# Optimization experiments

Measured on AMD Instinct MI355X. Metric: run time of the kernel, lower is better.

Reference implementation:

```python
import jax, jax.numpy as jnp
import numpy as np

K = 16          # neighbors per point
POINTNUM = 2048 # opt.pointnum
B, N = 8, 2048


def _knn_concat(x, k):
    """x: [B,N,C] -> [B,N,k,2C] = concat(center, k-nearest neighbor feats)."""
    sq = jnp.sum(x * x, axis=-1)                                   # [B,N]
    d2 = sq[:, :, None] + sq[:, None, :] - 2.0 * jnp.einsum('bnc,bmc->bnm', x, x)
    _, idx = jax.lax.top_k(-d2, k)                                 # [B,N,k]
    nbr = jax.vmap(lambda xb, ib: xb[ib])(x, idx)                  # [B,N,k,C]
    ctr = jnp.broadcast_to(x[:, :, None, :], nbr.shape)
    return jnp.concatenate([ctr, nbr], axis=-1)


def _lin(x, w, b):
    return x @ w + b


lrelu = jax.nn.leaky_relu  # default negative_slope=0.01 matches nn.LeakyReLU()


def setup_inputs() -> dict:
    key = jax.random.key(0)
    ks = jax.random.split(key, 20)

    def w(k_, fi, fo):
        return jax.random.normal(k_, (fi, fo), jnp.float32) / np.sqrt(fi)

    inp = {
        'x': jax.random.normal(ks[0], (B, N, 3), jnp.float32),
        'h1w1': w(ks[1], 6, 16),   'h1b1': jnp.zeros((16,), jnp.float32),
        'h1w2': w(ks[2], 16, 64),  'h1b2': jnp.zeros((64,), jnp.float32),
        'h1w3': w(ks[3], 64, 32),  'h1b3': jnp.zeros((32,), jnp.float32),
        'h2w1': w(ks[4], 64, 256), 'h2b1': jnp.zeros((256,), jnp.float32),
        'h2w2': w(ks[5], 256, 128),'h2b2': jnp.zeros((128,), jnp.float32),
        'h3w1': w(ks[6], 256, 128),'h3b1': jnp.zeros((128,), jnp.float32),
        'fc1w': w(ks[7], 128, 128),'fc1b': jnp.zeros((128,), jnp.float32),
        'fc2w': w(ks[8], 128, 128),'fc2b': jnp.zeros((128,), jnp.float32),
        'fc3w': w(ks[9], 128, POINTNUM * 3), 'fc3b': jnp.zeros((POINTNUM * 3,), jnp.float32),
    }
    return inp


def reference(x, h1w1, h1b1, h1w2, h1b2, h1w3, h1b3,
              h2w1, h2b1, h2w2, h2b2, h3w1, h3b1,
              fc1w, fc1b, fc2w, fc2b, fc3w, fc3b):
    # block 1: knn-concat [B,N,K,6] -> MLP(6,16,64,32) -> sum over K
    x1 = _knn_concat(x, K)
    h = lrelu(_lin(x1, h1w1, h1b1))
    h = lrelu(_lin(h, h1w2, h1b2))
    h = lrelu(_lin(h, h1w3, h1b3))
    x2 = jnp.sum(h, axis=2)                    # [B,N,32]
    # block 2: [B,N,K,64] -> MLP(64,256,128) -> sum over K
    x2 = _knn_concat(x2, K)
    h = lrelu(_lin(x2, h2w1, h2b1))
    h = lrelu(_lin(h, h2w2, h2b2))
    x3 = jnp.sum(h, axis=2)                    # [B,N,128]
    # block 3: [B,N,K,256] -> MLP(256,128) -> sum over K
    x3 = _knn_concat(x3, K)
    h = lrelu(_lin(x3, h3w1, h3b1))
    x4 = jnp.sum(h, axis=2)                    # [B,N,128]
    # global max pool over points
    x5 = jnp.max(x4, axis=1)                   # [B,128]
    x6 = lrelu(_lin(x5, fc1w, fc1b))
    x7 = lrelu(_lin(x6, fc2w, fc2b))
    x8 = _lin(x7, fc3w, fc3b)                  # [B, POINTNUM*3]
    return x8.reshape(x8.shape[0], POINTNUM, 3)
```

## Files before the change

### kernel.cpp

```cpp
#include <hip/hip_runtime.h>

#define KNB 16
#define BSZ 8
#define NPT 2048

typedef __attribute__((ext_vector_type(8))) short bf16x8;
typedef __attribute__((ext_vector_type(4))) float f32x4;

__device__ __forceinline__ float lrelu(float x) { return x >= 0.f ? x : 0.01f * x; }

__device__ __forceinline__ unsigned short bf16rne(float f) {
    union { float f; unsigned int u; } v; v.f = f;
    return (unsigned short)((v.u + 0x7FFFu + ((v.u >> 16) & 1u)) >> 16);
}

__device__ __forceinline__ float packkey(float d, int idx) {
    union { float f; unsigned int u; } v; v.f = d;
    v.u = (v.u & 0xFFFFF800u) | (unsigned int)idx;
    return v.f;
}

__device__ __forceinline__ void ceA(float& a, float& b) {
    const float lo = fminf(a, b), hi = fmaxf(a, b);
    a = lo; b = hi;
}

__device__ __forceinline__ void bsort16(float* c) {
#pragma unroll
    for (int k = 2; k <= 16; k <<= 1) {
#pragma unroll
        for (int j = k >> 1; j > 0; j >>= 1) {
#pragma unroll
            for (int i = 0; i < 16; ++i) {
                const int l = i ^ j;
                if (l > i) {
                    if ((i & k) == 0) ceA(c[i], c[l]);
                    else              ceA(c[l], c[i]);
                }
            }
        }
    }
}

__device__ __forceinline__ void merge16(float* L, const float* C) {
#pragma unroll
    for (int i = 0; i < 16; ++i) L[i] = fminf(L[i], C[15 - i]);
#pragma unroll
    for (int j = 8; j > 0; j >>= 1) {
#pragma unroll
        for (int i = 0; i < 16; ++i) {
            const int l = i ^ j;
            if (l > i) ceA(L[i], L[l]);
        }
    }
}

__device__ __forceinline__ void st16(float* dst, const float* L) {
#pragma unroll
    for (int c = 0; c < 4; ++c)
        *(f32x4*)(dst + c * 4) = (f32x4){L[c * 4], L[c * 4 + 1], L[c * 4 + 2], L[c * 4 + 3]};
}

__device__ __forceinline__ void ld16(float* L, const float* src) {
#pragma unroll
    for (int c = 0; c < 4; ++c) {
        const f32x4 v = *(const f32x4*)(src + c * 4);
        L[c * 4] = v[0]; L[c * 4 + 1] = v[1]; L[c * 4 + 2] = v[2]; L[c * 4 + 3] = v[3];
    }
}

__device__ __forceinline__ void xwave_merge_out(float (*sS)[20], int w, int lane,
                                                float* L, float* outp) {
    st16(sS[w * 64 + lane], L);
    __syncthreads();
    if ((w & 1) == 0) {
        float C[16];
        ld16(C, sS[(w + 1) * 64 + lane]);
        merge16(L, C);
        if (w == 2) st16(sS[2 * 64 + lane], L);
    }
    __syncthreads();
    if (w == 0) {
        float C[16];
        ld16(C, sS[2 * 64 + lane]);
        merge16(L, C);
        st16(outp, L);
    }
}

__global__ void wprep_kernel(const float* __restrict__ w, unsigned short* __restrict__ wt,
                             int K, int N) {
    int i = blockIdx.x * 256 + threadIdx.x;
    if (i < K * N) { int k = i / N, n = i - k * N; wt[n * K + k] = bf16rne(w[i]); }
}

__global__ void wprep_b1_kernel(const float* __restrict__ w1, const float* __restrict__ w2,
                                const float* __restrict__ w3,
                                unsigned short* __restrict__ w1a, unsigned short* __restrict__ w2a,
                                unsigned short* __restrict__ w3a) {
    int i = blockIdx.x * 256 + threadIdx.x;
    if (i < 512) {
        int n = i >> 5, k = i & 31;
        w1a[i] = (k < 6) ? bf16rne(w1[k * 16 + n]) : (unsigned short)0;
    } else if (i < 2560) {
        int j = i - 512, n = j >> 5, k = j & 31;
        w2a[j] = (k < 16) ? bf16rne(w2[k * 64 + n]) : (unsigned short)0;
    } else if (i < 4608) {
        int j = i - 2560, n = j >> 6, k = j & 63;
        w3a[j] = bf16rne(w3[k * 32 + n]);
    }
}

template<int C>
__global__ void norms16_kernel(const unsigned short* __restrict__ feat, float* __restrict__ out) {
    int gid = blockIdx.x * blockDim.x + threadIdx.x;
    if (gid < BSZ * NPT) {
        const unsigned short* p = feat + (size_t)gid * C;
        float s = 0.f;
#pragma unroll
        for (int c = 0; c < C; ++c) {
            union { unsigned int u; float f; } v; v.u = ((unsigned int)p[c]) << 16;
            s = fmaf(v.f, v.f, s);
        }
        out[gid] = s;
    }
}

template<int C>
__global__ void norms_kernel(const float* __restrict__ feat, float* __restrict__ out) {
    int gid = blockIdx.x * blockDim.x + threadIdx.x;
    if (gid < BSZ * NPT) {
        const float* p = feat + (size_t)gid * C;
        float s = 0.f;
#pragma unroll
        for (int c = 0; c < C; ++c) s = fmaf(p[c], p[c], s);
        out[gid] = s;
    }
}

template<int JS>
__launch_bounds__(256, 3)
__global__ void knn3_kernel(const float* __restrict__ feat,
                            const float* __restrict__ norms,
                            float* __restrict__ cand) {
    constexpr int JL = NPT / JS;
    constexpr int JP = JL / 4;
    const int b = blockIdx.z, js = blockIdx.y, i0 = blockIdx.x * 64;
    const int t = threadIdx.x, w = t >> 6, lane = t & 63;
    const float* fb = feat + (size_t)b * NPT * 3;
    const float* nb = norms + (size_t)b * NPT;

    __shared__ __align__(16) float sS[256][20];

    float q0, q1, q2;
    { const float* qp = fb + (size_t)(i0 + lane) * 3; q0 = qp[0]; q1 = qp[1]; q2 = qp[2]; }

    float L[16];
#pragma unroll
    for (int u = 0; u < 16; ++u) L[u] = 3e38f;

    const int jbeg = js * JL + w * JP;
#pragma unroll 1
    for (int j0 = jbeg; j0 < jbeg + JP; j0 += 16) {
        float C[16];
#pragma unroll
        for (int u = 0; u < 16; ++u) {
            const int j = j0 + u;
            const float* pp = fb + (size_t)j * 3;
            C[u] = packkey(fmaf(-2.f, fmaf(q0, pp[0], fmaf(q1, pp[1], q2 * pp[2])), nb[j]), j);
        }
        bsort16(C);
        merge16(L, C);
    }
    float* o = cand + (((size_t)b * NPT + i0 + lane) * JS + js) * 16;
    xwave_merge_out(sS, w, lane, L, o);
}

template<int C, int JS>
__launch_bounds__(256, 3)
__global__ void knn_mfma_kernel(const unsigned short* __restrict__ fb16,
                                const float* __restrict__ norms,
                                float* __restrict__ cand) {
    constexpr int JL = NPT / JS;
    constexpr int KS = C / 32;
    const int b    = blockIdx.z;
    const int js   = blockIdx.y;
    const int i0   = blockIdx.x * 64;
    const int t    = threadIdx.x;
    const int w    = t >> 6;
    const int lane = t & 63;
    const int l15  = lane & 15;
    const int quad = lane >> 4;
    const unsigned short* fbb = fb16 + (size_t)b * NPT * C;
    const float* nb = norms + (size_t)b * NPT;

    __shared__ __align__(16) float sS[256][20];

    bf16x8 afr[KS * 4];
#pragma unroll
    for (int ks = 0; ks < KS; ++ks)
#pragma unroll
        for (int mi = 0; mi < 4; ++mi)
            afr[ks * 4 + mi] = *(const bf16x8*)(fbb + (size_t)(i0 + mi * 16 + l15) * C + ks * 32 + quad * 8);

    float L[16];
#pragma unroll
    for (int u = 0; u < 16; ++u) L[u] = 3e38f;

    const int jbeg = js * JL;
#pragma unroll 1
    for (int j0 = jbeg; j0 < jbeg + JL; j0 += 64) {
        f32x4 acc[4];
#pragma unroll
        for (int mi = 0; mi < 4; ++mi) acc[mi] = (f32x4){0.f, 0.f, 0.f, 0.f};
        const unsigned short* prow = fbb + (size_t)(j0 + w * 16 + l15) * C + quad * 8;
#pragma unroll
        for (int ks = 0; ks < KS; ++ks) {
            const bf16x8 bfr = *(const bf16x8*)(prow + ks * 32);
#pragma unroll
            for (int mi = 0; mi < 4; ++mi)
                acc[mi] = __builtin_amdgcn_mfma_f32_16x16x32_bf16(afr[ks * 4 + mi], bfr, acc[mi], 0, 0, 0);
        }
        const float nv  = nb[j0 + w * 16 + l15];
        const int  cidx = j0 + w * 16 + l15;
#pragma unroll
        for (int mi = 0; mi < 4; ++mi)
#pragma unroll
            for (int r = 0; r < 4; ++r)
                sS[w * 64 + mi * 16 + quad * 4 + r][l15] = packkey(fmaf(-2.f, acc[mi][r], nv), cidx);
        float Cb[16];
        ld16(Cb, sS[w * 64 + lane]);
        bsort16(Cb);
        merge16(L, Cb);
    }

    float* o = cand + (((size_t)b * NPT + i0 + lane) * JS + js) * 16;
    xwave_merge_out(sS, w, lane, L, o);
}

template<int JS>
__launch_bounds__(256)
__global__ void knn_merge_kernel(const float* __restrict__ cand, int* __restrict__ knn_out) {
    const int q = blockIdx.x * 256 + threadIdx.x;
    const float* pd = cand + (size_t)q * JS * 16;
    float L[16];
    ld16(L, pd);
#pragma unroll
    for (int s = 1; s < JS; ++s) {
        float C[16];
        ld16(C, pd + s * 16);
        merge16(L, C);
    }
    int* o = knn_out + (size_t)q * KNB;
#pragma unroll
    for (int u = 0; u < 16; ++u) {
        union { float f; unsigned int v; } z; z.f = L[u];
        o[u] = (int)(z.v & 2047u);
    }
}

__launch_bounds__(256, 3)
__global__ void block1_mfma_kernel(const float* __restrict__ x, const int* __restrict__ knn,
                                   const unsigned short* __restrict__ w1a, const float* __restrict__ b1,
                                   const unsigned short* __restrict__ w2a, const float* __restrict__ b2,
                                   const unsigned short* __restrict__ w3a, const float* __restrict__ b3,
                                   unsigned short* __restrict__ x2b) {
    const int w = threadIdx.x >> 6, lane = threadIdx.x & 63;
    const int l15 = lane & 15, quad = lane >> 4;

    const bf16x8 W1 = *(const bf16x8*)(w1a + l15 * 32 + quad * 8);
    bf16x8 W2[4];
#pragma unroll
    for (int nt = 0; nt < 4; ++nt)
        W2[nt] = *(const bf16x8*)(w2a + (nt * 16 + l15) * 32 + quad * 8);
    bf16x8 W3[2][2];
#pragma unroll
    for (int tt = 0; tt < 2; ++tt)
#pragma unroll
        for (int ks = 0; ks < 2; ++ks)
            W3[tt][ks] = *(const bf16x8*)(w3a + (tt * 16 + l15) * 64 + ks * 32 + quad * 8);
    float b1v[4], b2v[4][4], b3v[2][4];
#pragma unroll
    for (int r = 0; r < 4; ++r) b1v[r] = b1[quad * 4 + r];
#pragma unroll
    for (int nt = 0; nt < 4; ++nt)
#pragma unroll
        for (int r = 0; r < 4; ++r) b2v[nt][r] = b2[nt * 16 + quad * 4 + r];
#pragma unroll
    for (int tt = 0; tt < 2; ++tt)
#pragma unroll
        for (int r = 0; r < 4; ++r) b3v[tt][r] = b3[tt * 16 + quad * 4 + r];

    const int src0 = ((2 * quad) & 3) * 16 + l15;
    const int src1 = ((2 * quad + 1) & 3) * 16 + l15;
    const int ntsel = quad >> 1;

    const int p0 = blockIdx.x * 16 + w * 4;
#pragma unroll 1
    for (int pi = 0; pi < 4; ++pi) {
        const int p = p0 + pi, b = p >> 11, n = p & (NPT - 1);
        int d0 = 0, d1 = 0, d2 = 0;
        if (quad == 0) {
            const float* xc = x + ((size_t)b * NPT + n) * 3;
            const int jn = knn[(size_t)p * KNB + l15];
            const float* xn = x + ((size_t)b * NPT + jn) * 3;
            const unsigned s0 = bf16rne(xc[0]), s1 = bf16rne(xc[1]), s2 = bf16rne(xc[2]);
            const unsigned s3 = bf16rne(xn[0]), s4 = bf16rne(xn[1]), s5 = bf16rne(xn[2]);
            d0 = (int)(s0 | (s1 << 16));
            d1 = (int)(s2 | (s3 << 16));
            d2 = (int)(s4 | (s5 << 16));
        }
        union { int i[4]; bf16x8 v; } B1;
        B1.i[0] = d0; B1.i[1] = d1; B1.i[2] = d2; B1.i[3] = 0;
        const f32x4 a1 = __builtin_amdgcn_mfma_f32_16x16x32_bf16(W1, B1.v, (f32x4){0.f, 0.f, 0.f, 0.f}, 0, 0, 0);

        int h10, h11;
        {
            const unsigned t0 = bf16rne(lrelu(a1[0] + b1v[0]));
            const unsigned t1 = bf16rne(lrelu(a1[1] + b1v[1]));
            const unsigned t2 = bf16rne(lrelu(a1[2] + b1v[2]));
            const unsigned t3 = bf16rne(lrelu(a1[3] + b1v[3]));
            h10 = (int)(t0 | (t1 << 16));
            h11 = (int)(t2 | (t3 << 16));
        }
        union { int i[4]; bf16x8 v; } B2;
        {
            const int e0 = __shfl(h10, src0), e1 = __shfl(h11, src0);
            const int e2 = __shfl(h10, src1), e3 = __shfl(h11, src1);
            const bool val = quad < 2;
            B2.i[0] = val ? e0 : 0; B2.i[1] = val ? e1 : 0;
            B2.i[2] = val ? e2 : 0; B2.i[3] = val ? e3 : 0;
        }
        f32x4 a2[4];
#pragma unroll
        for (int nt = 0; nt < 4; ++nt)
            a2[nt] = __builtin_amdgcn_mfma_f32_16x16x32_bf16(W2[nt], B2.v, (f32x4){0.f, 0.f, 0.f, 0.f}, 0, 0, 0);
        int dpk[4][2];
#pragma unroll
        for (int nt = 0; nt < 4; ++nt) {
            const unsigned t0 = bf16rne(lrelu(a2[nt][0] + b2v[nt][0]));
            const unsigned t1 = bf16rne(lrelu(a2[nt][1] + b2v[nt][1]));
            const unsigned t2 = bf16rne(lrelu(a2[nt][2] + b2v[nt][2]));
            const unsigned t3 = bf16rne(lrelu(a2[nt][3] + b2v[nt][3]));
            dpk[nt][0] = (int)(t0 | (t1 << 16));
            dpk[nt][1] = (int)(t2 | (t3 << 16));
        }
        f32x4 a3[2] = { (f32x4){0.f, 0.f, 0.f, 0.f}, (f32x4){0.f, 0.f, 0.f, 0.f} };
#pragma unroll
        for (int ks = 0; ks < 2; ++ks) {
            union { int i[4]; bf16x8 v; } B3;
            const int a0l = __shfl(dpk[2 * ks][0], src0), a0h = __shfl(dpk[2 * ks + 1][0], src0);
            const int a1l = __shfl(dpk[2 * ks][1], src0), a1h = __shfl(dpk[2 * ks + 1][1], src0);
            const int a2l = __shfl(dpk[2 * ks][0], src1), a2h = __shfl(dpk[2 * ks + 1][0], src1);
            const int a3l = __shfl(dpk[2 * ks][1], src1), a3h = __shfl(dpk[2 * ks + 1][1], src1);
            B3.i[0] = ntsel ? a0h : a0l;
            B3.i[1] = ntsel ? a1h : a1l;
            B3.i[2] = ntsel ? a2h : a2l;
            B3.i[3] = ntsel ? a3h : a3l;
#pragma unroll
            for (int tt = 0; tt < 2; ++tt)
                a3[tt] = __builtin_amdgcn_mfma_f32_16x16x32_bf16(W3[tt][ks], B3.v, a3[tt], 0, 0, 0);
        }
#pragma unroll
        for (int tt = 0; tt < 2; ++tt) {
#pragma unroll
            for (int r = 0; r < 4; ++r) {
                float s = lrelu(a3[tt][r] + b3v[tt][r]);
                s += __shfl_xor(s, 1);
                s += __shfl_xor(s, 2);
                s += __shfl_xor(s, 4);
                s += __shfl_xor(s, 8);
                if (l15 == 0)
                    x2b[(size_t)p * 32 + tt * 16 + quad * 4 + r] = bf16rne(s);
            }
        }
    }
}

__launch_bounds__(256, 2)
__global__ void block2_fused_kernel(const unsigned short* __restrict__ x2b,
                                    const int* __restrict__ knn,
                                    const unsigned short* __restrict__ w1t,
                                    const float* __restrict__ b1,
                                    const unsigned short* __restrict__ w2t,
                                    const float* __restrict__ b2,
                                    unsigned short* __restrict__ x3b) {
    const int w    = threadIdx.x >> 6;
    const int lane = threadIdx.x & 63;
    const int l15  = lane & 15, quad = lane >> 4;
    __shared__ __align__(16) unsigned short sH1[2][16][264];

    bf16x8 B1[4][2];
#pragma unroll
    for (int nt2 = 0; nt2 < 4; ++nt2)
#pragma unroll
        for (int ks = 0; ks < 2; ++ks)
            B1[nt2][ks] = *(const bf16x8*)(w1t + (size_t)(w * 64 + nt2 * 16 + l15) * 64 + ks * 32 + quad * 8);
    bf16x8 B2[2][8];
#pragma unroll
    for (int nt2 = 0; nt2 < 2; ++nt2)
#pragma unroll
        for (int ks = 0; ks < 8; ++ks)
            B2[nt2][ks] = *(const bf16x8*)(w2t + (size_t)(w * 32 + nt2 * 16 + l15) * 256 + ks * 32 + quad * 8);
    float b1v[4];
#pragma unroll
    for (int nt2 = 0; nt2 < 4; ++nt2) b1v[nt2] = b1[w * 64 + nt2 * 16 + l15];
    float b2v[2];
#pragma unroll
    for (int nt2 = 0; nt2 < 2; ++nt2) b2v[nt2] = b2[w * 32 + nt2 * 16 + l15];

    const int p0 = blockIdx.x * 8;
#pragma unroll 1
    for (int pi = 0; pi < 8; ++pi) {
        const int p = p0 + pi, b = p >> 11, buf = pi & 1;
        const int nbr = knn[(size_t)p * KNB + l15];
        const bf16x8 a0 = *(const bf16x8*)(x2b + (size_t)p * 32 + quad * 8);
        const bf16x8 a1 = *(const bf16x8*)(x2b + ((size_t)(b * NPT) + nbr) * 32 + quad * 8);
#pragma unroll
        for (int nt2 = 0; nt2 < 4; ++nt2) {
            f32x4 acc = (f32x4){0.f, 0.f, 0.f, 0.f};
            acc = __builtin_amdgcn_mfma_f32_16x16x32_bf16(a0, B1[nt2][0], acc, 0, 0, 0);
            acc = __builtin_amdgcn_mfma_f32_16x16x32_bf16(a1, B1[nt2][1], acc, 0, 0, 0);
#pragma unroll
            for (int r = 0; r < 4; ++r)
                sH1[buf][quad * 4 + r][w * 64 + nt2 * 16 + l15] = bf16rne(lrelu(acc[r] + b1v[nt2]));
        }
        __syncthreads();
        bf16x8 af[8];
#pragma unroll
        for (int ks = 0; ks < 8; ++ks)
            af[ks] = *(const bf16x8*)&sH1[buf][l15][ks * 32 + quad * 8];
#pragma unroll
        for (int nt2 = 0; nt2 < 2; ++nt2) {
            f32x4 acc = (f32x4){0.f, 0.f, 0.f, 0.f};
#pragma unroll
            for (int ks = 0; ks < 8; ++ks)
                acc = __builtin_amdgcn_mfma_f32_16x16x32_bf16(af[ks], B2[nt2][ks], acc, 0, 0, 0);
            float s = 0.f;
#pragma unroll
            for (int r = 0; r < 4; ++r) s += lrelu(acc[r] + b2v[nt2]);
            s += __shfl_xor(s, 16);
            s += __shfl_xor(s, 32);
            if (quad == 0) x3b[(size_t)p * 128 + w * 32 + nt2 * 16 + l15] = bf16rne(s);
        }
    }
}

__launch_bounds__(256, 3)
__global__ void block3_fused_kernel(const unsigned short* __restrict__ x3b,
                                    const int* __restrict__ knn,
                                    const unsigned short* __restrict__ w3t,
                                    const float* __restrict__ bias,
                                    float* __restrict__ x4) {
    const int w    = threadIdx.x >> 6;
    const int lane = threadIdx.x & 63;
    const int l15  = lane & 15, quad = lane >> 4;

    bf16x8 B3[2][8];
#pragma unroll
    for (int nt2 = 0; nt2 < 2; ++nt2)
#pragma unroll
        for (int ks = 0; ks < 8; ++ks)
            B3[nt2][ks] = *(const bf16x8*)(w3t + (size_t)(w * 32 + nt2 * 16 + l15) * 256 + ks * 32 + quad * 8);
    float bv[2];
#pragma unroll
    for (int nt2 = 0; nt2 < 2; ++nt2) bv[nt2] = bias[w * 32 + nt2 * 16 + l15];

    const int p0 = blockIdx.x * 8;
#pragma unroll 1
    for (int pi = 0; pi < 8; ++pi) {
        const int p = p0 + pi, b = p >> 11;
        const int nbr = knn[(size_t)p * KNB + l15];
        const unsigned short* ctr = x3b + (size_t)p * 128 + quad * 8;
        const unsigned short* nbp = x3b + ((size_t)(b * NPT) + nbr) * 128 + quad * 8;
        bf16x8 af[8];
#pragma unroll
        for (int ks = 0; ks < 4; ++ks) af[ks] = *(const bf16x8*)(ctr + ks * 32);
#pragma unroll
        for (int ks = 0; ks < 4; ++ks) af[4 + ks] = *(const bf16x8*)(nbp + ks * 32);
#pragma unroll
        for (int nt2 = 0; nt2 < 2; ++nt2) {
            f32x4 acc = (f32x4){0.f, 0.f, 0.f, 0.f};
#pragma unroll
            for (int ks = 0; ks < 8; ++ks)
                acc = __builtin_amdgcn_mfma_f32_16x16x32_bf16(af[ks], B3[nt2][ks], acc, 0, 0, 0);
            float s = 0.f;
#pragma unroll
            for (int r = 0; r < 4; ++r) s += lrelu(acc[r] + bv[nt2]);
            s += __shfl_xor(s, 16);
            s += __shfl_xor(s, 32);
            if (quad == 0) x4[(size_t)p * 128 + w * 32 + nt2 * 16 + l15] = s;
        }
    }
}

__launch_bounds__(128)
__global__ void maxpool_partial_kernel(const float* __restrict__ x4,
                                       float* __restrict__ part) {
    const int chunk = blockIdx.x, b = blockIdx.y, t = threadIdx.x;
    const float* xb = x4 + ((size_t)b * NPT + (size_t)chunk * 128) * 128;
    float m = -1e30f;
#pragma unroll 8
    for (int n = 0; n < 128; ++n) m = fmaxf(m, xb[(size_t)n * 128 + t]);
    part[((size_t)b * 16 + chunk) * 128 + t] = m;
}

__launch_bounds__(128)
__global__ void head2_kernel(const float* __restrict__ part,
                             const float* __restrict__ fc1w, const float* __restrict__ fc1b,
                             const float* __restrict__ fc2w, const float* __restrict__ fc2b,
                             const float* __restrict__ fc3w, const float* __restrict__ fc3b,
                             float* __restrict__ out) {
    const int g = blockIdx.x, b = blockIdx.y, t = threadIdx.x;
    __shared__ float s5[128], s6[128], s7[128];
    float m = -1e30f;
#pragma unroll
    for (int c = 0; c < 16; ++c)
        m = fmaxf(m, part[((size_t)b * 16 + c) * 128 + t]);
    s5[t] = m;
    __syncthreads();
    float a = fc1b[t];
#pragma unroll 4
    for (int i = 0; i < 128; ++i) a = fmaf(s5[i], fc1w[i * 128 + t], a);
    s6[t] = lrelu(a);
    __syncthreads();
    a = fc2b[t];
#pragma unroll 4
    for (int i = 0; i < 128; ++i) a = fmaf(s6[i], fc2w[i * 128 + t], a);
    s7[t] = lrelu(a);
    __syncthreads();
    const int o = g * 128 + t;
    float acc = fc3b[o];
#pragma unroll 4
    for (int i = 0; i < 128; ++i) acc = fmaf(s7[i], fc3w[(size_t)i * 6144 + o], acc);
    out[(size_t)b * 6144 + o] = acc;
}

extern "C" void kernel_launch(void* const* d_in, const int* in_sizes, int n_in,
                              void* d_out, int out_size, void* d_ws, size_t ws_size,
                              hipStream_t stream) {
    const float* x    = (const float*)d_in[0];
    const float* h1w1 = (const float*)d_in[1];
    const float* h1b1 = (const float*)d_in[2];
    const float* h1w2 = (const float*)d_in[3];
    const float* h1b2 = (const float*)d_in[4];
    const float* h1w3 = (const float*)d_in[5];
    const float* h1b3 = (const float*)d_in[6];
    const float* h2w1 = (const float*)d_in[7];
    const float* h2b1 = (const float*)d_in[8];
    const float* h2w2 = (const float*)d_in[9];
    const float* h2b2 = (const float*)d_in[10];
    const float* h3w1 = (const float*)d_in[11];
    const float* h3b1 = (const float*)d_in[12];
    const float* fc1w = (const float*)d_in[13];
    const float* fc1b = (const float*)d_in[14];
    const float* fc2w = (const float*)d_in[15];
    const float* fc2b = (const float*)d_in[16];
    const float* fc3w = (const float*)d_in[17];
    const float* fc3b = (const float*)d_in[18];

    float* ws = (float*)d_ws;
    unsigned short* x2b16 = (unsigned short*)ws;
    unsigned short* x3b16 = (unsigned short*)(ws + 262144);
    float* x4   = ws + 1310720;
    int*   idx  = (int*)(ws + 3407872);
    float* nrm  = ws + 3670016;
    float* part = ws + 3686400;
    unsigned short* w1t = (unsigned short*)(ws + 3702784);
    unsigned short* w2t = (unsigned short*)(ws + 3710976);
    unsigned short* w3t = (unsigned short*)(ws + 3727360);
    unsigned short* w1a = (unsigned short*)(ws + 3743744);
    unsigned short* w2a = (unsigned short*)(ws + 3744000);
    unsigned short* w3a = (unsigned short*)(ws + 3745024);
    float* cd   = ws + 3746048;
    float* out  = (float*)d_out;

    const dim3 kg(32, 4, 8);

    wprep_kernel<<<64, 256, 0, stream>>>(h2w1, w1t, 64, 256);
    wprep_kernel<<<128, 256, 0, stream>>>(h2w2, w2t, 256, 128);
    wprep_kernel<<<128, 256, 0, stream>>>(h3w1, w3t, 256, 128);
    wprep_b1_kernel<<<18, 256, 0, stream>>>(h1w1, h1w2, h1w3, w1a, w2a, w3a);

    norms_kernel<3><<<64, 256, 0, stream>>>(x, nrm);
    knn3_kernel<4><<<kg, 256, 0, stream>>>(x, nrm, cd);
    knn_merge_kernel<4><<<64, 256, 0, stream>>>(cd, idx);
    block1_mfma_kernel<<<1024, 256, 0, stream>>>(x, idx, w1a, h1b1, w2a, h1b2, w3a, h1b3, x2b16);

    norms16_kernel<32><<<64, 256, 0, stream>>>(x2b16, nrm);
    knn_mfma_kernel<32, 4><<<kg, 256, 0, stream>>>(x2b16, nrm, cd);
    knn_merge_kernel<4><<<64, 256, 0, stream>>>(cd, idx);
    block2_fused_kernel<<<BSZ * NPT / 8, 256, 0, stream>>>(x2b16, idx, w1t, h2b1, w2t, h2b2, x3b16);

    norms16_kernel<128><<<64, 256, 0, stream>>>(x3b16, nrm);
    knn_mfma_kernel<128, 4><<<kg, 256, 0, stream>>>(x3b16, nrm, cd);
    knn_merge_kernel<4><<<64, 256, 0, stream>>>(cd, idx);
    block3_fused_kernel<<<BSZ * NPT / 8, 256, 0, stream>>>(x3b16, idx, w3t, h3b1, x4);

    maxpool_partial_kernel<<<dim3(16, 8), 128, 0, stream>>>(x4, part);
    head2_kernel<<<dim3(48, 8), 128, 0, stream>>>(part, fc1w, fc1b, fc2w, fc2b,
                                                  fc3w, fc3b, out);
}
```

Before: 374.4 us.

## Software-pipeline gather loads in block2/block3 kernels and vectorize norm loads

```diff
diff --git a/kernel.cpp b/kernel.cpp
--- a/kernel.cpp
+++ b/kernel.cpp
@@ -118,9 +118,14 @@
         const unsigned short* p = feat + (size_t)gid * C;
         float s = 0.f;
 #pragma unroll
-        for (int c = 0; c < C; ++c) {
-            union { unsigned int u; float f; } v; v.u = ((unsigned int)p[c]) << 16;
-            s = fmaf(v.f, v.f, s);
+        for (int c8 = 0; c8 < C / 8; ++c8) {
+            const bf16x8 v = *(const bf16x8*)(p + c8 * 8);
+#pragma unroll
+            for (int j = 0; j < 8; ++j) {
+                union { unsigned int u; float f; } t;
+                t.u = ((unsigned int)(unsigned short)v[j]) << 16;
+                s = fmaf(t.f, t.f, s);
+            }
         }
         out[gid] = s;
     }
@@ -296,7 +301,7 @@
     const int ntsel = quad >> 1;
 
     const int p0 = blockIdx.x * 16 + w * 4;
-#pragma unroll 1
+#pragma unroll 2
     for (int pi = 0; pi < 4; ++pi) {
         const int p = p0 + pi, b = p >> 11, n = p & (NPT - 1);
         int d0 = 0, d1 = 0, d2 = 0;
@@ -410,12 +415,13 @@
     for (int nt2 = 0; nt2 < 2; ++nt2) b2v[nt2] = b2[w * 32 + nt2 * 16 + l15];
 
     const int p0 = blockIdx.x * 8;
-#pragma unroll 1
-    for (int pi = 0; pi < 8; ++pi) {
-        const int p = p0 + pi, b = p >> 11, buf = pi & 1;
-        const int nbr = knn[(size_t)p * KNB + l15];
-        const bf16x8 a0 = *(const bf16x8*)(x2b + (size_t)p * 32 + quad * 8);
-        const bf16x8 a1 = *(const bf16x8*)(x2b + ((size_t)(b * NPT) + nbr) * 32 + quad * 8);
+    const unsigned short* xb = x2b + (size_t)(p0 >> 11) * NPT * 32;
+
+    int nbrv[8];
+#pragma unroll
+    for (int pi = 0; pi < 8; ++pi) nbrv[pi] = knn[(size_t)(p0 + pi) * KNB + l15];
+
+    auto L1 = [&](const bf16x8& a0, const bf16x8& a1, int wbuf) {
 #pragma unroll
         for (int nt2 = 0; nt2 < 4; ++nt2) {
             f32x4 acc = (f32x4){0.f, 0.f, 0.f, 0.f};
@@ -423,9 +429,10 @@
             acc = __builtin_amdgcn_mfma_f32_16x16x32_bf16(a1, B1[nt2][1], acc, 0, 0, 0);
 #pragma unroll
             for (int r = 0; r < 4; ++r)
-                sH1[buf][quad * 4 + r][w * 64 + nt2 * 16 + l15] = bf16rne(lrelu(acc[r] + b1v[nt2]));
-        }
-        __syncthreads();
+                sH1[wbuf][quad * 4 + r][w * 64 + nt2 * 16 + l15] = bf16rne(lrelu(acc[r] + b1v[nt2]));
+        }
+    };
+    auto L2 = [&](int p, int buf) {
         bf16x8 af[8];
 #pragma unroll
         for (int ks = 0; ks < 8; ++ks)
@@ -442,6 +449,30 @@
             s += __shfl_xor(s, 16);
             s += __shfl_xor(s, 32);
             if (quad == 0) x3b[(size_t)p * 128 + w * 32 + nt2 * 16 + l15] = bf16rne(s);
+        }
+    };
+
+    bf16x8 a0A = *(const bf16x8*)(x2b + (size_t)p0 * 32 + quad * 8);
+    bf16x8 a1A = *(const bf16x8*)(xb + (size_t)nbrv[0] * 32 + quad * 8);
+    bf16x8 a0B = *(const bf16x8*)(x2b + (size_t)(p0 + 1) * 32 + quad * 8);
+    bf16x8 a1B = *(const bf16x8*)(xb + (size_t)nbrv[1] * 32 + quad * 8);
+    L1(a0A, a1A, 0);
+
+#pragma unroll
+    for (int pj = 0; pj < 4; ++pj) {
+        __syncthreads();
+        L2(p0 + 2 * pj, 0);
+        if (pj < 3) {
+            a0A = *(const bf16x8*)(x2b + (size_t)(p0 + 2 * pj + 2) * 32 + quad * 8);
+            a1A = *(const bf16x8*)(xb + (size_t)nbrv[2 * pj + 2] * 32 + quad * 8);
+        }
+        L1(a0B, a1B, 1);
+        __syncthreads();
+        L2(p0 + 2 * pj + 1, 1);
+        if (pj < 3) {
+            a0B = *(const bf16x8*)(x2b + (size_t)(p0 + 2 * pj + 3) * 32 + quad * 8);
+            a1B = *(const bf16x8*)(xb + (size_t)nbrv[2 * pj + 3] * 32 + quad * 8);
+            L1(a0A, a1A, 0);
         }
     }
 }
@@ -467,17 +498,21 @@
     for (int nt2 = 0; nt2 < 2; ++nt2) bv[nt2] = bias[w * 32 + nt2 * 16 + l15];
 
     const int p0 = blockIdx.x * 8;
-#pragma unroll 1
-    for (int pi = 0; pi < 8; ++pi) {
-        const int p = p0 + pi, b = p >> 11;
-        const int nbr = knn[(size_t)p * KNB + l15];
-        const unsigned short* ctr = x3b + (size_t)p * 128 + quad * 8;
-        const unsigned short* nbp = x3b + ((size_t)(b * NPT) + nbr) * 128 + quad * 8;
-        bf16x8 af[8];
+    const unsigned short* xb = x3b + (size_t)(p0 >> 11) * NPT * 128;
+
+    int nbrv[8];
+#pragma unroll
+    for (int pi = 0; pi < 8; ++pi) nbrv[pi] = knn[(size_t)(p0 + pi) * KNB + l15];
+
+    auto LDAF = [&](bf16x8* af, int pi, int nbr) {
+        const unsigned short* ctr = x3b + (size_t)(p0 + pi) * 128 + quad * 8;
+        const unsigned short* nbp = xb + (size_t)nbr * 128 + quad * 8;
 #pragma unroll
         for (int ks = 0; ks < 4; ++ks) af[ks] = *(const bf16x8*)(ctr + ks * 32);
 #pragma unroll
         for (int ks = 0; ks < 4; ++ks) af[4 + ks] = *(const bf16x8*)(nbp + ks * 32);
+    };
+    auto CMP = [&](int p, const bf16x8* af) {
 #pragma unroll
         for (int nt2 = 0; nt2 < 2; ++nt2) {
             f32x4 acc = (f32x4){0.f, 0.f, 0.f, 0.f};
@@ -491,6 +526,16 @@
             s += __shfl_xor(s, 32);
             if (quad == 0) x4[(size_t)p * 128 + w * 32 + nt2 * 16 + l15] = s;
         }
+    };
+
+    bf16x8 afA[8], afB[8];
+    LDAF(afA, 0, nbrv[0]);
+#pragma unroll
+    for (int pj = 0; pj < 4; ++pj) {
+        LDAF(afB, 2 * pj + 1, nbrv[2 * pj + 1]);
+        CMP(p0 + 2 * pj, afA);
+        if (pj < 3) LDAF(afA, 2 * pj + 2, nbrv[2 * pj + 2]);
+        CMP(p0 + 2 * pj + 1, afB);
     }
 }
 
```

Result: no change. 376.1 us (+0.5%).
